# Kernel optimization log

Hardware: AMD Instinct MI355X
Metric: run time of the kernel (lower is better)

## Reference

```python
import jax, jax.numpy as jnp
import numpy as np

N = 65536      # nodes (256x256 grid)
E = 1048576    # edges (avg degree 16)
T_IN = 10      # TIME_STEPS_IN
L = 64         # LATENT_DIMS
MID = 128      # LATENT_DIMS * MLP_RATIO
GD = 2         # grid dims


def _lin_init(key, fan_in, fan_out):
    kw, kb = jax.random.split(key)
    s = 1.0 / np.sqrt(fan_in)
    W = jax.random.uniform(kw, (fan_in, fan_out), jnp.float32, -s, s)
    b = jax.random.uniform(kb, (fan_out,), jnp.float32, -s, s)
    return W, b


def setup_inputs() -> dict:
    key = jax.random.key(0)
    ks = jax.random.split(key, 10)
    x = jax.random.normal(ks[0], (N, T_IN), jnp.float32)
    grid = jax.random.uniform(ks[1], (N, GD), jnp.float32)
    edge_index = jax.random.randint(ks[2], (2, E), 0, N, jnp.int64)
    W_proj1, b_proj1 = _lin_init(ks[3], T_IN + GD, MID)
    W_proj2, b_proj2 = _lin_init(ks[4], MID, L)
    Wk, bk = _lin_init(ks[5], 2 * L + 2 * GD + 1, L)   # K edge MLP (single linear)
    Ww, bw = _lin_init(ks[6], L, L)                     # W node MLP (single linear)
    W_dec1, b_dec1 = _lin_init(ks[7], L, MID)
    W_dec2, b_dec2 = _lin_init(ks[8], MID, 1)
    return {"x": x, "grid": grid, "edge_index": edge_index,
            "W_proj1": W_proj1, "b_proj1": b_proj1, "W_proj2": W_proj2, "b_proj2": b_proj2,
            "Wk": Wk, "bk": bk, "Ww": Ww, "bw": bw,
            "W_dec1": W_dec1, "b_dec1": b_dec1, "W_dec2": W_dec2, "b_dec2": b_dec2}


def _gelu(x):
    return jax.nn.gelu(x, approximate=False)  # torch F.gelu default = exact erf


def reference(x, grid, edge_index, W_proj1, b_proj1, W_proj2, b_proj2,
              Wk, bk, Ww, bw, W_dec1, b_dec1, W_dec2, b_dec2):
    # project: cat(x, grid) -> Linear -> GELU -> Linear
    h = jnp.concatenate([x, grid], axis=-1)               # [N, T_IN+2]
    h = _gelu(h @ W_proj1 + b_proj1) @ W_proj2 + b_proj2  # [N, L]

    # message passing block (PyG source_to_target: j = row 0, i = row 1)
    src = edge_index[0]
    dst = edge_index[1]
    x_j = h[src]                                          # [E, L]
    x_i = h[dst]                                          # [E, L]
    g_j = grid[src]                                       # [E, 2]
    g_i = grid[dst]                                       # [E, 2]
    dist = jnp.sqrt(jnp.sum(jnp.square(g_i - g_j), axis=-1, keepdims=True))  # [E, 1]
    ef = jnp.concatenate([dist, g_i, g_j, x_i, x_j], axis=-1)  # [E, 2L+5]
    msg = ef @ Wk + bk                                    # [E, L]
    aggr = jax.ops.segment_sum(msg, dst, num_segments=N)  # [N, L]
    h = _gelu(h @ Ww + bw + aggr)                         # update

    # decode: Linear -> GELU -> Linear
    out = _gelu(h @ W_dec1 + b_dec1) @ W_dec2 + b_dec2    # [N, 1]
    return out
```

## Files before the change

### kernel.cpp

```cpp
#include <hip/hip_runtime.h>
#include <hip/hip_fp16.h>

static __device__ __forceinline__ float gelu(float x) {
    return 0.5f * x * (1.0f + erff(x * 0.70710678118654752f));
}

#define CAPR 32

typedef _Float16 v8h __attribute__((ext_vector_type(8)));
typedef float    v4f __attribute__((ext_vector_type(4)));
union F8 { uint4 u; v8h v; _Float16 f[8]; };

static __device__ __forceinline__ void acc8(float* a, uint4 u) {
    float2 f0 = __half22float2(*(__half2*)&u.x);
    float2 f1 = __half22float2(*(__half2*)&u.y);
    float2 f2 = __half22float2(*(__half2*)&u.z);
    float2 f3 = __half22float2(*(__half2*)&u.w);
    a[0] += f0.x; a[1] += f0.y; a[2] += f1.x; a[3] += f1.y;
    a[4] += f2.x; a[5] += f2.y; a[6] += f3.x; a[7] += f3.y;
}

static __device__ __forceinline__ uint4 pack8(const float* v) {
    __half2 p0 = __floats2half2_rn(v[0], v[1]);
    __half2 p1 = __floats2half2_rn(v[2], v[3]);
    __half2 p2 = __floats2half2_rn(v[4], v[5]);
    __half2 p3 = __floats2half2_rn(v[6], v[7]);
    uint4 u;
    u.x = *(unsigned*)&p0; u.y = *(unsigned*)&p1;
    u.z = *(unsigned*)&p2; u.w = *(unsigned*)&p3;
    return u;
}

__global__ void __launch_bounds__(256, 1)
k_enc_scat(const float* __restrict__ x,
           const float* __restrict__ grid,
           const float* __restrict__ W1,
           const float* __restrict__ b1,
           const float* __restrict__ W2,
           const float* __restrict__ b2,
           const int* __restrict__ ei, int* __restrict__ cnt,
           int* __restrict__ ssrc,
           __half* __restrict__ h16, int N, int E, int scatB)
{
    __shared__ uint4 tabW1[512];
    __shared__ uint4 tabW2[1024];
    __shared__ __half wmids[4 * 16 * 136];
    int tid = threadIdx.x;

    if ((int)blockIdx.x < scatB) {
        int e4 = blockIdx.x * 256 + tid;
        const int4* s4 = (const int4*)ei;
        const int4* d4 = (const int4*)(ei + E);
        int4 s = s4[e4];
        int4 d = d4[e4];
        int p;
        p = atomicAdd(&cnt[(d.x << 1) + 0], 1); if (p < CAPR) ssrc[((size_t)d.x << 6) + p] = s.x;
        p = atomicAdd(&cnt[(d.y << 1) + 1], 1); if (p < CAPR) ssrc[((size_t)d.y << 6) + 32 + p] = s.y;
        p = atomicAdd(&cnt[(d.z << 1) + 0], 1); if (p < CAPR) ssrc[((size_t)d.z << 6) + p] = s.z;
        p = atomicAdd(&cnt[(d.w << 1) + 1], 1); if (p < CAPR) ssrc[((size_t)d.w << 6) + 32 + p] = s.w;
        return;
    }

    int eb = blockIdx.x - scatB;
    for (int idx = tid; idx < 512; idx += 256) {
        int lane = idx & 63, nt = idx >> 6;
        int col = nt * 16 + (lane & 15);
        int k0 = (lane >> 4) << 3;
        F8 f;
#pragma unroll
        for (int j = 0; j < 8; j++)
            f.f[j] = (k0 + j < 12) ? (_Float16)W1[(k0 + j) * 128 + col] : (_Float16)0.f;
        tabW1[idx] = f.u;
    }
    for (int idx = tid; idx < 1024; idx += 256) {
        int lane = idx & 63, nt = (idx >> 6) & 3, kc = idx >> 8;
        int col = nt * 16 + (lane & 15);
        int k0 = kc * 32 + ((lane >> 4) << 3);
        F8 f;
#pragma unroll
        for (int j = 0; j < 8; j++) f.f[j] = (_Float16)W2[(k0 + j) * 64 + col];
        tabW2[idx] = f.u;
    }
    __syncthreads();

    int lane = tid & 63, wave = tid >> 6;
    int m = lane & 15, quad = lane >> 4;
    __half* wm = &wmids[wave * 16 * 136];

    for (int t = 0; t < 2; t++) {
        int tile = eb * 8 + wave * 2 + t;
        int base = tile * 16;
        int n = base + m;
        F8 a1;
#pragma unroll
        for (int j = 0; j < 8; j++) a1.f[j] = (_Float16)0.f;
        if (quad == 0) {
            float2 x0 = *(const float2*)&x[(size_t)n * 10 + 0];
            float2 x1 = *(const float2*)&x[(size_t)n * 10 + 2];
            float2 x2 = *(const float2*)&x[(size_t)n * 10 + 4];
            float2 x3 = *(const float2*)&x[(size_t)n * 10 + 6];
            a1.f[0] = (_Float16)x0.x; a1.f[1] = (_Float16)x0.y;
            a1.f[2] = (_Float16)x1.x; a1.f[3] = (_Float16)x1.y;
            a1.f[4] = (_Float16)x2.x; a1.f[5] = (_Float16)x2.y;
            a1.f[6] = (_Float16)x3.x; a1.f[7] = (_Float16)x3.y;
        } else if (quad == 1) {
            float2 x4 = *(const float2*)&x[(size_t)n * 10 + 8];
            float2 g  = *(const float2*)&grid[(size_t)n * 2];
            a1.f[0] = (_Float16)x4.x; a1.f[1] = (_Float16)x4.y;
            a1.f[2] = (_Float16)g.x;  a1.f[3] = (_Float16)g.y;
        }
#pragma unroll
        for (int nt = 0; nt < 8; nt++) {
            int col = nt * 16 + m;
            float b = b1[col];
            v4f acc = {b, b, b, b};
            F8 bf; bf.u = tabW1[nt * 64 + lane];
            acc = __builtin_amdgcn_mfma_f32_16x16x32_f16(a1.v, bf.v, acc, 0, 0, 0);
#pragma unroll
            for (int reg = 0; reg < 4; reg++)
                wm[(quad * 4 + reg) * 136 + col] = __float2half(gelu(acc[reg]));
        }
        __syncthreads();

        F8 a2[4];
#pragma unroll
        for (int kc = 0; kc < 4; kc++)
            a2[kc].u = *(const uint4*)&wm[m * 136 + kc * 32 + quad * 8];
#pragma unroll
        for (int nt = 0; nt < 4; nt++) {
            int col = nt * 16 + m;
            float b = b2[col];
            v4f acc = {b, b, b, b};
#pragma unroll
            for (int kc = 0; kc < 4; kc++) {
                F8 bf; bf.u = tabW2[kc * 256 + nt * 64 + lane];
                acc = __builtin_amdgcn_mfma_f32_16x16x32_f16(a2[kc].v, bf.v, acc, 0, 0, 0);
            }
#pragma unroll
            for (int reg = 0; reg < 4; reg++)
                h16[(size_t)(base + quad * 4 + reg) * 64 + col] = __float2half(acc[reg]);
        }
        __syncthreads();
    }
}

__global__ void k_gather(const __half* __restrict__ h16,
                         const float* __restrict__ grid,
                         const int* __restrict__ ssrc, const int* __restrict__ cnt,
                         __half* __restrict__ sum_h16, float* __restrict__ sum_g,
                         float* __restrict__ sum_d, int N)
{
    int tid = blockIdx.x * blockDim.x + threadIdx.x;
    int n = tid >> 3;
    int l = tid & 7;
    if (n >= N) return;
    int2 cv = *(const int2*)&cnt[n << 1];
    const uint4* h8 = (const uint4*)h16;
    float a[8] = {0,0,0,0,0,0,0,0};
    float sgx = 0.f, sgy = 0.f, sd = 0.f;
    float gix = grid[2 * n], giy = grid[2 * n + 1];
#pragma unroll
    for (int r = 0; r < 2; r++) {
        int dg = min((r == 0) ? cv.x : cv.y, CAPR);
        const int* sr = ssrc + ((size_t)n << 6) + r * 32;
        int i = 0;
        for (; i + 3 < dg; i += 4) {
            int4 s = *(const int4*)&sr[i];
            uint4 u0 = h8[(size_t)s.x * 8 + l];
            uint4 u1 = h8[(size_t)s.y * 8 + l];
            uint4 u2 = h8[(size_t)s.z * 8 + l];
            uint4 u3 = h8[(size_t)s.w * 8 + l];
            acc8(a, u0); acc8(a, u1); acc8(a, u2); acc8(a, u3);
            if (l < 4) {
                int sj = (l == 0) ? s.x : (l == 1) ? s.y : (l == 2) ? s.z : s.w;
                float2 g = *(const float2*)&grid[2 * sj];
                float dx = gix - g.x, dy = giy - g.y;
                sd += sqrtf(dx * dx + dy * dy);
                sgx += g.x; sgy += g.y;
            }
        }
        for (; i < dg; i++) {
            int s0 = sr[i];
            uint4 u0 = h8[(size_t)s0 * 8 + l];
            acc8(a, u0);
            if (l == 0) {
                float2 g = *(const float2*)&grid[2 * s0];
                float dx = gix - g.x, dy = giy - g.y;
                sd += sqrtf(dx * dx + dy * dy);
                sgx += g.x; sgy += g.y;
            }
        }
    }
    sd  += __shfl_xor(sd, 1);  sd  += __shfl_xor(sd, 2);  sd  += __shfl_xor(sd, 4);
    sgx += __shfl_xor(sgx, 1); sgx += __shfl_xor(sgx, 2); sgx += __shfl_xor(sgx, 4);
    sgy += __shfl_xor(sgy, 1); sgy += __shfl_xor(sgy, 2); sgy += __shfl_xor(sgy, 4);
    ((uint4*)(sum_h16 + (size_t)n * 64))[l] = pack8(a);
    if (l == 0) { sum_d[n] = sd; sum_g[2 * n] = sgx; sum_g[2 * n + 1] = sgy; }
}

__global__ void __launch_bounds__(256, 1)
k_update(const __half* __restrict__ h16, __half* __restrict__ sum_h16,
         const float* __restrict__ sum_g, const float* __restrict__ sum_d,
         const int* __restrict__ cnt, const float* __restrict__ grid,
         const float* __restrict__ Wk, const float* __restrict__ bk,
         const float* __restrict__ Ww, const float* __restrict__ bw, int N)
{
    __shared__ uint4 tabW[512];
    __shared__ uint4 tabC[512];
    __shared__ uint4 tabD[512];
    __shared__ uint4 tabV[256];
    int tid = threadIdx.x;

    for (int idx = tid; idx < 512; idx += 256) {
        int lane = idx & 63, nt = (idx >> 6) & 3, kc = idx >> 8;
        int col = nt * 16 + (lane & 15);
        int kr  = kc * 32 + ((lane >> 4) << 3);
        F8 fw, fc, fd;
#pragma unroll
        for (int j = 0; j < 8; j++) {
            fw.f[j] = (_Float16)Ww[(kr + j) * 64 + col];
            fc.f[j] = (_Float16)Wk[(size_t)(5 + kr + j) * 64 + col];
            fd.f[j] = (_Float16)Wk[(size_t)(69 + kr + j) * 64 + col];
        }
        tabW[idx] = fw.u; tabC[idx] = fc.u; tabD[idx] = fd.u;
    }
    if (tid < 256) {
        int lane = tid & 63, nt = tid >> 6;
        int col = nt * 16 + (lane & 15);
        F8 fv;
#pragma unroll
        for (int j = 0; j < 8; j++) fv.f[j] = (_Float16)0.f;
        if ((lane >> 4) == 0) {
            fv.f[0] = (_Float16)bw[col];
            fv.f[1] = (_Float16)bk[col];
            fv.f[2] = (_Float16)Wk[col];
            fv.f[3] = (_Float16)Wk[64 + col];
            fv.f[4] = (_Float16)Wk[128 + col];
            fv.f[5] = (_Float16)Wk[192 + col];
            fv.f[6] = (_Float16)Wk[256 + col];
        }
        tabV[tid] = fv.u;
    }
    __syncthreads();

    int lane = tid & 63, wave = tid >> 6;
    int m = lane & 15, quad = lane >> 4;
    const uint4* h8 = (const uint4*)h16;
    const uint4* s8 = (const uint4*)sum_h16;

    for (int t = 0; t < 2; t++) {
        int tile = blockIdx.x * 8 + wave * 2 + t;
        int base = tile * 16;
        int n = base + m;
        int2 cv = *(const int2*)&cnt[n << 1];
        float deg = (float)(min(cv.x, CAPR) + min(cv.y, CAPR));
        float sd  = sum_d[n];
        float sgx = sum_g[2 * n], sgy = sum_g[2 * n + 1];
        float gix = grid[2 * n] * deg, giy = grid[2 * n + 1] * deg;

        F8 ah0, ah1, as0, as1, ahd0, ahd1, au;
        ah0.u = h8[(size_t)n * 8 + quad];
        ah1.u = h8[(size_t)n * 8 + 4 + quad];
        as0.u = s8[(size_t)n * 8 + quad];
        as1.u = s8[(size_t)n * 8 + 4 + quad];
        _Float16 dh = (_Float16)deg;
#pragma unroll
        for (int j = 0; j < 8; j++) { ahd0.f[j] = ah0.f[j] * dh; ahd1.f[j] = ah1.f[j] * dh; }
        float z = (quad == 0) ? 1.f : 0.f;
        au.f[0] = (_Float16)z;          au.f[1] = (_Float16)(deg * z);
        au.f[2] = (_Float16)(sd * z);   au.f[3] = (_Float16)(gix * z);
        au.f[4] = (_Float16)(giy * z);  au.f[5] = (_Float16)(sgx * z);
        au.f[6] = (_Float16)(sgy * z);  au.f[7] = (_Float16)0.f;

        float h2v[4][4];
#pragma unroll
        for (int nt = 0; nt < 4; nt++) {
            F8 bv, bw0, bw1, bc0, bc1, bd0, bd1f;
            bv.u  = tabV[nt * 64 + lane];
            bw0.u = tabW[nt * 64 + lane];       bw1.u = tabW[256 + nt * 64 + lane];
            bc0.u = tabC[nt * 64 + lane];       bc1.u = tabC[256 + nt * 64 + lane];
            bd0.u = tabD[nt * 64 + lane];       bd1f.u = tabD[256 + nt * 64 + lane];
            v4f acc = {0.f, 0.f, 0.f, 0.f};
            acc = __builtin_amdgcn_mfma_f32_16x16x32_f16(au.v,   bv.v,   acc, 0, 0, 0);
            acc = __builtin_amdgcn_mfma_f32_16x16x32_f16(ah0.v,  bw0.v,  acc, 0, 0, 0);
            acc = __builtin_amdgcn_mfma_f32_16x16x32_f16(ah1.v,  bw1.v,  acc, 0, 0, 0);
            acc = __builtin_amdgcn_mfma_f32_16x16x32_f16(ahd0.v, bc0.v,  acc, 0, 0, 0);
            acc = __builtin_amdgcn_mfma_f32_16x16x32_f16(ahd1.v, bc1.v,  acc, 0, 0, 0);
            acc = __builtin_amdgcn_mfma_f32_16x16x32_f16(as0.v,  bd0.v,  acc, 0, 0, 0);
            acc = __builtin_amdgcn_mfma_f32_16x16x32_f16(as1.v,  bd1f.v, acc, 0, 0, 0);
#pragma unroll
            for (int reg = 0; reg < 4; reg++) h2v[nt][reg] = gelu(acc[reg]);
        }
#pragma unroll
        for (int reg = 0; reg < 4; reg++) {
            int nr = base + quad * 4 + reg;
#pragma unroll
            for (int nt = 0; nt < 4; nt++)
                sum_h16[(size_t)nr * 64 + m + 16 * nt] = __float2half(h2v[nt][reg]);
        }
    }
}

__global__ void __launch_bounds__(256, 1)
k_decode(const __half* __restrict__ h2g,
         const float* __restrict__ Wd1, const float* __restrict__ bd1,
         const float* __restrict__ Wd2, const float* __restrict__ bd2,
         float* __restrict__ out, int N)
{
    __shared__ uint4 tab[1024];
    int tid = threadIdx.x;
    for (int idx = tid; idx < 1024; idx += 256) {
        int lane = idx & 63, nt = (idx >> 6) & 7, kc = idx >> 9;
        int col = nt * 16 + (lane & 15);
        int kr  = kc * 32 + ((lane >> 4) << 3);
        F8 f;
#pragma unroll
        for (int j = 0; j < 8; j++) f.f[j] = (_Float16)Wd1[(kr + j) * 128 + col];
        tab[idx] = f.u;
    }
    __syncthreads();

    int lane = tid & 63, wave = tid >> 6;
    int m = lane & 15, quad = lane >> 4;
    const uint4* h8 = (const uint4*)h2g;
    float bd2v = bd2[0];

    for (int t = 0; t < 2; t++) {
        int tile = blockIdx.x * 8 + wave * 2 + t;
        int base = tile * 16;
        int n = base + m;
        F8 ah0, ah1;
        ah0.u = h8[(size_t)n * 8 + quad];
        ah1.u = h8[(size_t)n * 8 + 4 + quad];
        float p[4] = {0.f, 0.f, 0.f, 0.f};
#pragma unroll
        for (int nt = 0; nt < 8; nt++) {
            int col = m + 16 * nt;
            float b = bd1[col];
            float w2 = Wd2[col];
            F8 b0, b1;
            b0.u = tab[nt * 64 + lane];
            b1.u = tab[512 + nt * 64 + lane];
            v4f acc = {b, b, b, b};
            acc = __builtin_amdgcn_mfma_f32_16x16x32_f16(ah0.v, b0.v, acc, 0, 0, 0);
            acc = __builtin_amdgcn_mfma_f32_16x16x32_f16(ah1.v, b1.v, acc, 0, 0, 0);
#pragma unroll
            for (int reg = 0; reg < 4; reg++) p[reg] += gelu(acc[reg]) * w2;
        }
#pragma unroll
        for (int reg = 0; reg < 4; reg++) {
            p[reg] += __shfl_xor(p[reg], 1);
            p[reg] += __shfl_xor(p[reg], 2);
            p[reg] += __shfl_xor(p[reg], 4);
            p[reg] += __shfl_xor(p[reg], 8);
        }
        if (m == 0) {
#pragma unroll
            for (int reg = 0; reg < 4; reg++)
                out[base + quad * 4 + reg] = p[reg] + bd2v;
        }
    }
}

extern "C" void kernel_launch(void* const* d_in, const int* in_sizes, int n_in,
                              void* d_out, int out_size, void* d_ws, size_t ws_size,
                              hipStream_t stream)
{
    const float* x    = (const float*)d_in[0];
    const float* grid = (const float*)d_in[1];
    const int*   ei   = (const int*)d_in[2];
    const float* W1   = (const float*)d_in[3];
    const float* b1   = (const float*)d_in[4];
    const float* W2   = (const float*)d_in[5];
    const float* b2   = (const float*)d_in[6];
    const float* Wk   = (const float*)d_in[7];
    const float* bk   = (const float*)d_in[8];
    const float* Ww   = (const float*)d_in[9];
    const float* bw   = (const float*)d_in[10];
    const float* Wd1  = (const float*)d_in[11];
    const float* bd1  = (const float*)d_in[12];
    const float* Wd2  = (const float*)d_in[13];
    const float* bd2  = (const float*)d_in[14];
    float* out = (float*)d_out;

    int N = in_sizes[0] / 10;
    int E = in_sizes[2] / 2;

    char* ws = (char*)d_ws;
    size_t o_h16  = 0;
    size_t o_sh16 = o_h16  + (size_t)N * 64 * 2;
    size_t o_sumg = o_sh16 + (size_t)N * 64 * 2;
    size_t o_sumd = o_sumg + (size_t)N * 2 * 4;
    size_t o_cnt  = o_sumd + (size_t)N * 4;
    size_t o_ssrc = o_cnt  + (size_t)N * 2 * 4;

    __half* h16     = (__half*)(ws + o_h16);
    __half* sum_h16 = (__half*)(ws + o_sh16);
    float* sum_g = (float*)(ws + o_sumg);
    float* sum_d = (float*)(ws + o_sumd);
    int*   cnt   = (int*)  (ws + o_cnt);
    int*   ssrc  = (int*)  (ws + o_ssrc);

    hipMemsetAsync(cnt, 0, (size_t)N * 2 * 4, stream);

    int scatB = E / (256 * 4);
    int encB  = (N / 16) / 8;
    k_enc_scat<<<dim3(scatB + encB), dim3(256), 0, stream>>>(x, grid, W1, b1, W2, b2,
                                                             ei, cnt, ssrc, h16, N, E, scatB);
    k_gather<<<dim3((N * 8 + 255) / 256), dim3(256), 0, stream>>>(h16, grid, ssrc, cnt,
                                                                   sum_h16, sum_g, sum_d, N);
    int tiles = N / 16;
    k_update<<<dim3(tiles / 8), dim3(256), 0, stream>>>(h16, sum_h16, sum_g, sum_d, cnt,
                                                        grid, Wk, bk, Ww, bw, N);
    k_decode<<<dim3(tiles / 8), dim3(256), 0, stream>>>(sum_h16, Wd1, bd1, Wd2, bd2, out, N);
}
```

Measured before the change: 213.4 us.

## Fuse update and decode kernels via LDS tile, predicate gather tail loop

Merges the node update and decoder MLP into one kernel. The GELU-updated hidden tile is staged in per-wave LDS and transposed into the MFMA A-operand layout, so the update no longer writes h2 to global memory and decode no longer reads it back. This also removes one kernel launch. The gather kernel's scalar remainder loop is folded into the 4-wide loop by duplicating indices and predicating the accumulation. The fusion adds LDS usage and block-wide syncs between the two MFMA stages.

```diff
diff --git a/kernel.cpp b/kernel.cpp
--- a/kernel.cpp
+++ b/kernel.cpp
@@ -162,16 +162,24 @@
 #pragma unroll
     for (int r = 0; r < 2; r++) {
         int dg = min((r == 0) ? cv.x : cv.y, CAPR);
-        const int* sr = ssrc + ((size_t)n << 6) + r * 32;
-        int i = 0;
-        for (; i + 3 < dg; i += 4) {
+        const int* sr = ssrc + ((size_t)n << 6) + (r << 5);
+        for (int i = 0; i < dg; i += 4) {
             int4 s = *(const int4*)&sr[i];
+            int rem = dg - i;
+            if (rem < 4) {
+                if (rem <= 1) s.y = s.x;
+                if (rem <= 2) s.z = s.x;
+                s.w = (rem <= 3) ? s.x : s.w;
+            }
             uint4 u0 = h8[(size_t)s.x * 8 + l];
             uint4 u1 = h8[(size_t)s.y * 8 + l];
             uint4 u2 = h8[(size_t)s.z * 8 + l];
             uint4 u3 = h8[(size_t)s.w * 8 + l];
-            acc8(a, u0); acc8(a, u1); acc8(a, u2); acc8(a, u3);
-            if (l < 4) {
+            acc8(a, u0);
+            if (rem > 1) acc8(a, u1);
+            if (rem > 2) acc8(a, u2);
+            if (rem > 3) acc8(a, u3);
+            if (l < 4 && i + l < dg) {
                 int sj = (l == 0) ? s.x : (l == 1) ? s.y : (l == 2) ? s.z : s.w;
                 float2 g = *(const float2*)&grid[2 * sj];
                 float dx = gix - g.x, dy = giy - g.y;
@@ -179,17 +187,6 @@
                 sgx += g.x; sgy += g.y;
             }
         }
-        for (; i < dg; i++) {
-            int s0 = sr[i];
-            uint4 u0 = h8[(size_t)s0 * 8 + l];
-            acc8(a, u0);
-            if (l == 0) {
-                float2 g = *(const float2*)&grid[2 * s0];
-                float dx = gix - g.x, dy = giy - g.y;
-                sd += sqrtf(dx * dx + dy * dy);
-                sgx += g.x; sgy += g.y;
-            }
-        }
     }
     sd  += __shfl_xor(sd, 1);  sd  += __shfl_xor(sd, 2);  sd  += __shfl_xor(sd, 4);
     sgx += __shfl_xor(sgx, 1); sgx += __shfl_xor(sgx, 2); sgx += __shfl_xor(sgx, 4);
@@ -199,16 +196,21 @@
 }
 
 __global__ void __launch_bounds__(256, 1)
-k_update(const __half* __restrict__ h16, __half* __restrict__ sum_h16,
-         const float* __restrict__ sum_g, const float* __restrict__ sum_d,
-         const int* __restrict__ cnt, const float* __restrict__ grid,
-         const float* __restrict__ Wk, const float* __restrict__ bk,
-         const float* __restrict__ Ww, const float* __restrict__ bw, int N)
+k_updec(const __half* __restrict__ h16, const __half* __restrict__ sum_h16,
+        const float* __restrict__ sum_g, const float* __restrict__ sum_d,
+        const int* __restrict__ cnt, const float* __restrict__ grid,
+        const float* __restrict__ Wk, const float* __restrict__ bk,
+        const float* __restrict__ Ww, const float* __restrict__ bw,
+        const float* __restrict__ Wd1, const float* __restrict__ bd1,
+        const float* __restrict__ Wd2, const float* __restrict__ bd2,
+        float* __restrict__ out, int N)
 {
     __shared__ uint4 tabW[512];
     __shared__ uint4 tabC[512];
     __shared__ uint4 tabD[512];
     __shared__ uint4 tabV[256];
+    __shared__ uint4 tabE[1024];
+    __shared__ __half h2t[4 * 16 * 72];
     int tid = threadIdx.x;
 
     for (int idx = tid; idx < 512; idx += 256) {
@@ -241,12 +243,23 @@
         }
         tabV[tid] = fv.u;
     }
+    for (int idx = tid; idx < 1024; idx += 256) {
+        int lane = idx & 63, nt = (idx >> 6) & 7, kc = idx >> 9;
+        int col = nt * 16 + (lane & 15);
+        int kr  = kc * 32 + ((lane >> 4) << 3);
+        F8 f;
+#pragma unroll
+        for (int j = 0; j < 8; j++) f.f[j] = (_Float16)Wd1[(kr + j) * 128 + col];
+        tabE[idx] = f.u;
+    }
     __syncthreads();
 
     int lane = tid & 63, wave = tid >> 6;
     int m = lane & 15, quad = lane >> 4;
     const uint4* h8 = (const uint4*)h16;
     const uint4* s8 = (const uint4*)sum_h16;
+    __half* wt = &h2t[wave * 16 * 72];
+    float bd2v = bd2[0];
 
     for (int t = 0; t < 2; t++) {
         int tile = blockIdx.x * 8 + wave * 2 + t;
@@ -272,7 +285,6 @@
         au.f[4] = (_Float16)(giy * z);  au.f[5] = (_Float16)(sgx * z);
         au.f[6] = (_Float16)(sgy * z);  au.f[7] = (_Float16)0.f;
 
-        float h2v[4][4];
 #pragma unroll
         for (int nt = 0; nt < 4; nt++) {
             F8 bv, bw0, bw1, bc0, bc1, bd0, bd1f;
@@ -289,49 +301,14 @@
             acc = __builtin_amdgcn_mfma_f32_16x16x32_f16(as0.v,  bd0.v,  acc, 0, 0, 0);
             acc = __builtin_amdgcn_mfma_f32_16x16x32_f16(as1.v,  bd1f.v, acc, 0, 0, 0);
 #pragma unroll
-            for (int reg = 0; reg < 4; reg++) h2v[nt][reg] = gelu(acc[reg]);
-        }
-#pragma unroll
-        for (int reg = 0; reg < 4; reg++) {
-            int nr = base + quad * 4 + reg;
-#pragma unroll
-            for (int nt = 0; nt < 4; nt++)
-                sum_h16[(size_t)nr * 64 + m + 16 * nt] = __float2half(h2v[nt][reg]);
-        }
-    }
-}
-
-__global__ void __launch_bounds__(256, 1)
-k_decode(const __half* __restrict__ h2g,
-         const float* __restrict__ Wd1, const float* __restrict__ bd1,
-         const float* __restrict__ Wd2, const float* __restrict__ bd2,
-         float* __restrict__ out, int N)
-{
-    __shared__ uint4 tab[1024];
-    int tid = threadIdx.x;
-    for (int idx = tid; idx < 1024; idx += 256) {
-        int lane = idx & 63, nt = (idx >> 6) & 7, kc = idx >> 9;
-        int col = nt * 16 + (lane & 15);
-        int kr  = kc * 32 + ((lane >> 4) << 3);
-        F8 f;
-#pragma unroll
-        for (int j = 0; j < 8; j++) f.f[j] = (_Float16)Wd1[(kr + j) * 128 + col];
-        tab[idx] = f.u;
-    }
-    __syncthreads();
-
-    int lane = tid & 63, wave = tid >> 6;
-    int m = lane & 15, quad = lane >> 4;
-    const uint4* h8 = (const uint4*)h2g;
-    float bd2v = bd2[0];
-
-    for (int t = 0; t < 2; t++) {
-        int tile = blockIdx.x * 8 + wave * 2 + t;
-        int base = tile * 16;
-        int n = base + m;
-        F8 ah0, ah1;
-        ah0.u = h8[(size_t)n * 8 + quad];
-        ah1.u = h8[(size_t)n * 8 + 4 + quad];
+            for (int reg = 0; reg < 4; reg++)
+                wt[(quad * 4 + reg) * 72 + m + 16 * nt] = __float2half(gelu(acc[reg]));
+        }
+        __syncthreads();
+
+        F8 dh0, dh1;
+        dh0.u = *(const uint4*)&wt[m * 72 + quad * 8];
+        dh1.u = *(const uint4*)&wt[m * 72 + 32 + quad * 8];
         float p[4] = {0.f, 0.f, 0.f, 0.f};
 #pragma unroll
         for (int nt = 0; nt < 8; nt++) {
@@ -339,11 +316,11 @@
             float b = bd1[col];
             float w2 = Wd2[col];
             F8 b0, b1;
-            b0.u = tab[nt * 64 + lane];
-            b1.u = tab[512 + nt * 64 + lane];
+            b0.u = tabE[nt * 64 + lane];
+            b1.u = tabE[512 + nt * 64 + lane];
             v4f acc = {b, b, b, b};
-            acc = __builtin_amdgcn_mfma_f32_16x16x32_f16(ah0.v, b0.v, acc, 0, 0, 0);
-            acc = __builtin_amdgcn_mfma_f32_16x16x32_f16(ah1.v, b1.v, acc, 0, 0, 0);
+            acc = __builtin_amdgcn_mfma_f32_16x16x32_f16(dh0.v, b0.v, acc, 0, 0, 0);
+            acc = __builtin_amdgcn_mfma_f32_16x16x32_f16(dh1.v, b1.v, acc, 0, 0, 0);
 #pragma unroll
             for (int reg = 0; reg < 4; reg++) p[reg] += gelu(acc[reg]) * w2;
         }
@@ -359,6 +336,7 @@
             for (int reg = 0; reg < 4; reg++)
                 out[base + quad * 4 + reg] = p[reg] + bd2v;
         }
+        __syncthreads();
     }
 }
 
@@ -410,7 +388,7 @@
     k_gather<<<dim3((N * 8 + 255) / 256), dim3(256), 0, stream>>>(h16, grid, ssrc, cnt,
                                                                    sum_h16, sum_g, sum_d, N);
     int tiles = N / 16;
-    k_update<<<dim3(tiles / 8), dim3(256), 0, stream>>>(h16, sum_h16, sum_g, sum_d, cnt,
-                                                        grid, Wk, bk, Ww, bw, N);
-    k_decode<<<dim3(tiles / 8), dim3(256), 0, stream>>>(sum_h16, Wd1, bd1, Wd2, bd2, out, N);
-}
+    k_updec<<<dim3(tiles / 8), dim3(256), 0, stream>>>(h16, sum_h16, sum_g, sum_d, cnt,
+                                                       grid, Wk, bk, Ww, bw,
+                                                       Wd1, bd1, Wd2, bd2, out, N);
+}
```

Result: no change. 211.0 us (median of 2 runs) (-1.2%).
